# Kernel optimization log

Measured on AMD Instinct MI355X. Metric: run time of the kernel, lower is better.

The kernel has to match this reference:

```python
import jax, jax.numpy as jnp
import numpy as np

B, N, T, H = 32, 512, 3, 8
F_IN, F_HID, F_OUT = 768, 64, 64
NEG_SLOPE = 0.2
NEG_INF = -1e9


def setup_inputs() -> dict:
    key = jax.random.key(0)
    ks = jax.random.split(key, 16)
    s = 0.05
    emb = jax.random.normal(ks[0], (B, N, F_IN), jnp.float32)
    adj = jax.random.randint(ks[1], (B, N, N), 0, 2).astype(jnp.int32)
    adj = adj.at[:, jnp.arange(N), jnp.arange(N)].set(1)  # self loops so no empty rows
    vt_idx = jax.random.randint(ks[2], (B, N), 0, T)
    v_types = jax.nn.one_hot(vt_idx, T, dtype=jnp.float32)
    # layer 1 GAT params: per-type weights [T,H,f_in,f_out]
    w1 = jax.random.normal(ks[3], (T, H, F_IN, F_HID), jnp.float32) * s
    a_src1 = jax.random.normal(ks[4], (H, F_HID), jnp.float32) * s
    a_dst1 = jax.random.normal(ks[5], (H, F_HID), jnp.float32) * s
    b1 = jnp.zeros((F_HID,), jnp.float32)
    # layer 2 GAT (single head, f_in = H*F_HID)
    w2 = jax.random.normal(ks[6], (T, 1, H * F_HID, F_OUT), jnp.float32) * s
    a_src2 = jax.random.normal(ks[7], (1, F_OUT), jnp.float32) * s
    a_dst2 = jax.random.normal(ks[8], (1, F_OUT), jnp.float32) * s
    b2 = jnp.zeros((F_OUT,), jnp.float32)
    # MLP classifier: fc1 d->3d, fc2 3d->d, fc3 d->2
    fc1_w = jax.random.normal(ks[9], (F_OUT, 3 * F_OUT), jnp.float32) * s
    fc1_b = jnp.zeros((3 * F_OUT,), jnp.float32)
    fc2_w = jax.random.normal(ks[10], (3 * F_OUT, F_OUT), jnp.float32) * s
    fc2_b = jnp.zeros((F_OUT,), jnp.float32)
    fc3_w = jax.random.normal(ks[11], (F_OUT, 2), jnp.float32) * s
    fc3_b = jnp.zeros((2,), jnp.float32)
    return dict(emb=emb, adj=adj, v_types=v_types,
                w1=w1, a_src1=a_src1, a_dst1=a_dst1, b1=b1,
                w2=w2, a_src2=a_src2, a_dst2=a_dst2, b2=b2,
                fc1_w=fc1_w, fc1_b=fc1_b, fc2_w=fc2_w, fc2_b=fc2_b,
                fc3_w=fc3_w, fc3_b=fc3_b)


def _leaky_relu(x):
    return jnp.where(x >= 0, x, NEG_SLOPE * x)


def _gat(h, adj_mask, vt, w, a_src, a_dst, bias):
    # h: [B,N,f_in], vt: [B,N,T] one-hot, w: [T,Hd,f_in,f_out]
    # per-type projection then select node's type
    hpt = jnp.einsum('bni,thio->bntho', h, w)          # [B,N,T,Hd,f_out]
    hp = jnp.einsum('bnt,bntho->bnho', vt, hpt)        # [B,N,Hd,f_out]
    src = jnp.einsum('bnho,ho->bhn', hp, a_src)        # [B,Hd,N]
    dst = jnp.einsum('bnho,ho->bhn', hp, a_dst)
    e = _leaky_relu(src[:, :, :, None] + dst[:, :, None, :])  # [B,Hd,N,N]
    e = jnp.where(adj_mask[:, None, :, :], e, NEG_INF)
    attn = jax.nn.softmax(e, axis=-1)                  # attn_dropout=0.0 -> identity
    out = jnp.einsum('bhnm,bmho->bhno', attn, hp) + bias
    return out                                         # [B,Hd,N,f_out]


def reference(emb, adj, v_types, w1, a_src1, a_dst1, b1,
              w2, a_src2, a_dst2, b2,
              fc1_w, fc1_b, fc2_w, fc2_b, fc3_w, fc3_b):
    adj_mask = adj > 0
    x = _gat(emb, adj_mask, v_types, w1, a_src1, a_dst1, b1)    # [B,H,N,F_HID]
    x = jnp.transpose(x, (0, 2, 1, 3)).reshape(B, N, H * F_HID)  # concat heads
    x = jax.nn.elu(x)                                            # dropout: eval mode (identity)
    x = _gat(x, adj_mask, v_types, w2, a_src2, a_dst2, b2)       # [B,1,N,F_OUT]
    x = jax.nn.elu(x)
    x = x[:, 0, :, :]                                            # squeeze head dim -> [B,N,F_OUT]
    left = x[:, 0, :]
    right = x[:, 1, :]
    v = left * right
    v = jax.nn.relu(v @ fc1_w + fc1_b)
    v = jax.nn.relu(v @ fc2_w + fc2_b)
    scores = v @ fc3_w + fc3_b
    return jax.nn.log_softmax(scores, axis=1)
```

## Files before the change

kernel.cpp:

```cpp
#include <hip/hip_runtime.h>

#define BB   32
#define NN   512
#define NH   8
#define FIN  768
#define FHID 64
#define NROWS (BB*NN)

typedef __attribute__((ext_vector_type(8))) short bf16x8;
typedef __attribute__((ext_vector_type(4))) short s16x4;
typedef __attribute__((ext_vector_type(4))) float f32x4;
typedef unsigned long long u64;
typedef unsigned short u16;
typedef long i64;

__device__ __forceinline__ float lrelu_f(float s){ return fmaxf(s, 0.2f*s); }
__device__ __forceinline__ float elu_f(float s){ return s > 0.f ? s : expm1f(s); }
__device__ __forceinline__ short f2bf(float f){
  unsigned u = __float_as_uint(f);
  return (short)((u + 0x7fffu + ((u >> 16) & 1u)) >> 16);
}
__device__ __forceinline__ float bf2f(short s){
  return __uint_as_float(((unsigned)(u16)s) << 16);
}
__device__ __forceinline__ unsigned cvt_pk_bf16(float lo, float hi){
  unsigned r;
  asm("v_cvt_pk_bf16_f32 %0, %1, %2" : "=v"(r) : "v"(lo), "v"(hi));
  return r;
}
__device__ __forceinline__ float exp2_fast(float x){
  float r;
  asm("v_exp_f32 %0, %1" : "=v"(r) : "v"(x));
  return r;
}
__device__ __forceinline__ unsigned cvt_pk_fp8(float lo, float hi){
  return (unsigned)__builtin_amdgcn_cvt_pk_fp8_f32(lo, hi, 0, false);
}
__device__ __forceinline__ void gll16(const void* g, void* l){
  __builtin_amdgcn_global_load_lds(
      (const __attribute__((address_space(1))) void*)g,
      (__attribute__((address_space(3))) void*)l, 16, 0, 0);
}

__global__ __launch_bounds__(256) void prep_kernel(
    const int* __restrict__ adj,
    u64* __restrict__ maskw)
{
  int row  = blockIdx.x * 4 + (threadIdx.x >> 6);
  int lane = threadIdx.x & 63;
  const int* arow = adj + (long)row * NN;
  #pragma unroll
  for (int w = 0; w < 8; ++w) {
    u64 bal = __ballot(arow[w*64 + lane] > 0);
    if (lane == 0) maskw[(long)row*8 + w] = bal;
  }
}

__global__ __launch_bounds__(256) void rowlist_kernel(
    const float* __restrict__ vt,
    int* __restrict__ rowlist, int* __restrict__ counts)
{
  __shared__ int lc[3];
  __shared__ int lbase[3];
  int tid = threadIdx.x;
  int row = blockIdx.x * 256 + tid;
  if (tid < 3) lc[tid] = 0;
  __syncthreads();
  const float* v = vt + (long)row*3;
  int t = v[1] > 0.5f ? 1 : (v[2] > 0.5f ? 2 : 0);
  int p = atomicAdd(&lc[t], 1);
  __syncthreads();
  if (tid < 3) lbase[tid] = atomicAdd(&counts[tid], lc[tid]);
  __syncthreads();
  rowlist[t*NROWS + lbase[t] + p] = row;
}

__global__ __launch_bounds__(256) void conv_w(
    const float* __restrict__ w1, const float* __restrict__ w2,
    u16* __restrict__ w1t, u16* __restrict__ w2t)
{
  __shared__ float tile[64][68];
  int bid = blockIdx.x, tid = threadIdx.x;
  const float* src; u16* dst; int K;
  if (bid < 24) { src = w1 + (long)bid*768*64; dst = w1t + (long)bid*64*768; K = 768; }
  else { int t = bid - 24; src = w2 + (long)t*512*64; dst = w2t + (long)t*64*512; K = 512; }
  int kq = blockIdx.y;
  int kstart = kq * (K >> 2), kend = kstart + (K >> 2);

  for (int k0 = kstart; k0 < kend; k0 += 64) {
    __syncthreads();
    #pragma unroll
    for (int i = 0; i < 4; ++i) {
      int kk = i*16 + (tid >> 4);
      int oo = (tid & 15) * 4;
      float4 v = *(const float4*)(src + (long)(k0 + kk)*64 + oo);
      *(float4*)&tile[kk][oo] = v;
    }
    __syncthreads();
    int o = tid >> 2, kp = (tid & 3) * 16;
    unsigned pk[8];
    #pragma unroll
    for (int j = 0; j < 8; ++j)
      pk[j] = cvt_pk_bf16(tile[kp + 2*j][o], tile[kp + 2*j + 1][o]);
    u16* d = dst + (long)o*K + k0 + kp;
    #pragma unroll
    for (int j = 0; j < 8; ++j) *(unsigned*)(d + 2*j) = pk[j];
    __syncthreads();
  }
}

__global__ __launch_bounds__(256) void retile_w1(
    const u16* __restrict__ w1t, u16* __restrict__ w1tt)
{
  int thb = blockIdx.x;
  int kiter = blockIdx.y;
  int t = thb >> 2, hb = thb & 3;
  int tid = threadIdx.x;
  u16* dst = w1tt + ((long)thb*24 + kiter)*4096;
  #pragma unroll
  for (int c = 0; c < 2; ++c) {
    int u = c*256 + tid;
    int kg = u >> 7, col = u & 127;
    int head = hb*2 + (col >> 6), o = col & 63;
    int k = kiter*32 + kg*8;
    const u16* s = w1t + (((long)t*8 + head)*64 + o)*768 + k;
    *(bf16x8*)(dst + u*8) = *(const bf16x8*)s;
  }
}

__global__ __launch_bounds__(256) void gemm1_mfma(
    const float* __restrict__ emb,
    const u16* __restrict__ w1tt,
    const int* __restrict__ rowlist, const int* __restrict__ counts,
    u16* __restrict__ hp1b)
{
  int i   = blockIdx.x;
  int t   = i / 352;
  int r   = i - t*352;
  int cnt = counts[t];
  int xcd = r & 7;
  int q   = r >> 3;
  int hb  = q & 3;
  int rb  = (q >> 2) * 8 + xcd;
  int r0  = rb * 64;
  if (r0 >= cnt) return;

  __shared__ short aT[2][4*66*8];
  __shared__ short bT[2][4096];
  __shared__ int rowsS[64];

  int tid = threadIdx.x;
  if (tid < 64) {
    int rr = r0 + tid;
    rowsS[tid] = (rr < cnt) ? rowlist[t*NROWS + rr] : -1;
  }
  __syncthreads();

  int ar = tid >> 2, ac = tid & 3;
  int sg = rowsS[ar]; if (sg < 0) sg = rowsS[0];
  const float* aP = emb + (long)sg*768;

  const u16* bBase = w1tt + ((long)(t*4 + hb)*24)*4096;

  int wv = tid >> 6, l = tid & 63;
  int wr = wv >> 1, wc = wv & 1;
  int l15 = l & 15, lg = l >> 4;

  int aw0 = (( (ac>>1)     )*66 + ar)*8 + (ac&1)*4;
  int aw1 = (( 2 + (ac>>1) )*66 + ar)*8 + (ac&1)*4;

  f32x4 acc[2][4];
  #pragma unroll
  for (int fr = 0; fr < 2; ++fr)
    #pragma unroll
    for (int cf = 0; cf < 4; ++cf) acc[fr][cf] = (f32x4){0.f,0.f,0.f,0.f};

  gll16(bBase + tid*8,        &bT[0][tid*8]);
  gll16(bBase + (256+tid)*8,  &bT[0][(256+tid)*8]);
  float4 rA0 = *(const float4*)(aP + ac*4);
  float4 rA1 = *(const float4*)(aP + 16 + ac*4);
  {
    unsigned lo0 = cvt_pk_bf16(rA0.x, rA0.y), hi0 = cvt_pk_bf16(rA0.z, rA0.w);
    unsigned lo1 = cvt_pk_bf16(rA1.x, rA1.y), hi1 = cvt_pk_bf16(rA1.z, rA1.w);
    *(uint2*)&aT[0][aw0] = make_uint2(lo0, hi0);
    *(uint2*)&aT[0][aw1] = make_uint2(lo1, hi1);
  }
  rA0 = *(const float4*)(aP + 32 + ac*4);
  rA1 = *(const float4*)(aP + 48 + ac*4);
  __syncthreads();

  int cur = 0;
  for (int kiter = 0; kiter < 24; ++kiter) {
    if (kiter < 23) {
      const u16* bsrc = bBase + (long)(kiter+1)*4096;
      gll16(bsrc + tid*8,       &bT[cur^1][tid*8]);
      gll16(bsrc + (256+tid)*8, &bT[cur^1][(256+tid)*8]);
    }
    bf16x8 af_[2], bf_[4];
    #pragma unroll
    for (int fr = 0; fr < 2; ++fr)
      af_[fr] = *(const bf16x8*)&aT[cur][(lg*66 + wr*32 + fr*16 + l15)*8];
    #pragma unroll
    for (int cf = 0; cf < 4; ++cf)
      bf_[cf] = *(const bf16x8*)&bT[cur][(lg*128 + wc*64 + cf*16 + l15)*8];
    #pragma unroll
    for (int fr = 0; fr < 2; ++fr)
      #pragma unroll
      for (int cf = 0; cf < 4; ++cf)
        acc[fr][cf] = __builtin_amdgcn_mfma_f32_16x16x32_bf16(af_[fr], bf_[cf], acc[fr][cf], 0, 0, 0);
    if (kiter < 23) {
      unsigned lo0 = cvt_pk_bf16(rA0.x, rA0.y), hi0 = cvt_pk_bf16(rA0.z, rA0.w);
      unsigned lo1 = cvt_pk_bf16(rA1.x, rA1.y), hi1 = cvt_pk_bf16(rA1.z, rA1.w);
      *(uint2*)&aT[cur^1][aw0] = make_uint2(lo0, hi0);
      *(uint2*)&aT[cur^1][aw1] = make_uint2(lo1, hi1);
      if (kiter < 22) {
        rA0 = *(const float4*)(aP + (kiter+2)*32 + ac*4);
        rA1 = *(const float4*)(aP + (kiter+2)*32 + 16 + ac*4);
      }
    }
    __syncthreads();
    cur ^= 1;
  }

  #pragma unroll
  for (int fr = 0; fr < 2; ++fr) {
    #pragma unroll
    for (int r4 = 0; r4 < 4; ++r4) {
      int rloc = wr*32 + fr*16 + lg*4 + r4;
      int rg = rowsS[rloc];
      if (rg < 0) continue;
      long obase = ((long)(rg >> 9) * 8) * 32768 + (long)(rg & 511) * 64;
      #pragma unroll
      for (int cf = 0; cf < 4; ++cf) {
        int c = wc*64 + cf*16 + l15;
        hp1b[obase + (long)(hb*2 + (c >> 6))*32768 + (c & 63)] = (u16)f2bf(acc[fr][cf][r4]);
      }
    }
  }
}

__global__ __launch_bounds__(256) void gemm2_mfma(
    const u16* __restrict__ xbf,
    const u16* __restrict__ w2t,
    const int* __restrict__ rowlist, const int* __restrict__ counts,
    float* __restrict__ hp2)
{
  int i   = blockIdx.x;
  int t   = i >> 8;
  int cnt = counts[t];
  int r0  = (i & 255) * 64;
  if (r0 >= cnt) return;

  __shared__ short aT[4*66*8];
  __shared__ short bT[4*66*8];
  __shared__ int rowsS[64];

  int tid = threadIdx.x;
  if (tid < 64) {
    int rr = r0 + tid;
    rowsS[tid] = (rr < cnt) ? rowlist[t*NROWS + rr] : -1;
  }
  __syncthreads();

  int ar = tid >> 2, ac = tid & 3;
  int sg = rowsS[ar]; if (sg < 0) sg = rowsS[0];
  long apart = ((long)(sg >> 9) * 8) * 32768 + (long)(sg & 511) * 64;

  int colb = tid >> 2, off = tid & 3;
  const u16* bP = w2t + ((long)t*64 + colb)*512;

  int wv = tid >> 6, l = tid & 63;
  int l15 = l & 15, lg = l >> 4;

  f32x4 acc[4];
  #pragma unroll
  for (int cf = 0; cf < 4; ++cf) acc[cf] = (f32x4){0.f,0.f,0.f,0.f};

  int ka0 = ac*8;
  bf16x8 ra = *(const bf16x8*)(xbf + apart + (long)(ka0 >> 6)*32768 + (ka0 & 63));
  bf16x8 rb = *(const bf16x8*)(bP + off*8);

  for (int k0 = 0; k0 < 512; k0 += 32) {
    __syncthreads();
    *(bf16x8*)&aT[(ac*66 + ar)*8]   = ra;
    *(bf16x8*)&bT[(off*66 + colb)*8] = rb;
    __syncthreads();
    if (k0 + 32 < 512) {
      int kn = k0 + 32 + ac*8;
      ra = *(const bf16x8*)(xbf + apart + (long)(kn >> 6)*32768 + (kn & 63));
      rb = *(const bf16x8*)(bP + k0 + 32 + off*8);
    }
    bf16x8 af, bfr[4];
    af = *(const bf16x8*)&aT[(lg*66 + wv*16 + l15)*8];
    #pragma unroll
    for (int cf = 0; cf < 4; ++cf)
      bfr[cf] = *(const bf16x8*)&bT[(lg*66 + cf*16 + l15)*8];
    #pragma unroll
    for (int cf = 0; cf < 4; ++cf)
      acc[cf] = __builtin_amdgcn_mfma_f32_16x16x32_bf16(af, bfr[cf], acc[cf], 0, 0, 0);
  }

  #pragma unroll
  for (int r4 = 0; r4 < 4; ++r4) {
    int rloc = wv*16 + lg*4 + r4;
    int rg = rowsS[rloc];
    if (rg < 0) continue;
    #pragma unroll
    for (int cf = 0; cf < 4; ++cf)
      hp2[(long)rg*64 + cf*16 + l15] = acc[cf][r4];
  }
}

__global__ __launch_bounds__(1024) void gat1_attn(
    const u16* __restrict__ hp1b, const u64* __restrict__ maskw,
    const float* __restrict__ a_src, const float* __restrict__ a_dst,
    const float* __restrict__ b1, u16* __restrict__ xbf)
{
  extern __shared__ char smc[];
  char*  hpTf = smc;
  char*  pSf  = smc + 33792;
  float* srcS = (float*)(smc + 67584);
  float* dstS = (float*)(smc + 69632);
  float* asS  = (float*)(smc + 71680);
  float* adS  = (float*)(smc + 71936);
  float* rcpS = (float*)(smc + 72192);

  const float LOG2E = 1.4426950408889634f;

  int bid = blockIdx.x;
  int bh = bid >> 1, qh = bid & 1;
  int b = bh >> 3, h = bh & 7;
  int tid = threadIdx.x;

  if (tid < 64) asS[tid] = a_src[h*64 + tid];
  else if (tid < 128) adS[tid - 64] = a_dst[h*64 + (tid - 64)];
  __syncthreads();

  {
    int m = tid >> 1, half = tid & 1;
    int koct = m >> 3, kin = m & 7;
    const u16* hpRow = hp1b + ((long)bh*NN + m)*64 + half*32;
    float ps = 0.f, pd = 0.f;
    #pragma unroll
    for (int qq = 0; qq < 4; ++qq) {
      bf16x8 hv = *(const bf16x8*)(hpRow + qq*8);
      int o0 = half*32 + qq*8;
      #pragma unroll
      for (int j = 0; j < 8; ++j) {
        float f = bf2f(hv[j]);
        ps += f * asS[o0 + j];
        pd += f * adS[o0 + j];
        hpTf[(koct*66 + o0 + j)*8 + kin] = (char)(cvt_pk_fp8(f, f) & 0xffu);
      }
    }
    ps += __shfl_xor(ps, 1);
    pd += __shfl_xor(pd, 1);
    if ((tid & 1) == 0) { srcS[m] = ps * LOG2E; dstS[m] = pd * LOG2E; }
  }
  __syncthreads();

  int wv = tid >> 6, lane = tid & 63;
  int l15 = lane & 15, lg = lane >> 4;
  int cgl = wv >> 2, nt = wv & 3;
  int o_out = nt*16 + l15;
  float bb  = b1[o_out];

  float2 dst2[4];
  #pragma unroll
  for (int jj = 0; jj < 4; ++jj)
    dst2[jj] = *(const float2*)&dstS[jj*128 + 2*lane];
  int wsel = lane >> 5;
  unsigned sh = (unsigned)((2*lane) & 63);
  int pbase = ((lane >> 2)*66)*8 + 2*(lane & 3);

  for (int s = 0; s < 4; ++s) {
    int sup = qh*4 + s;
    #pragma unroll
    for (int rr = 0; rr < 4; ++rr) {
      int rloc = wv*4 + rr;
      int row  = sup*64 + rloc;
      float srcv = srcS[row];
      const u64* mrow = maskw + ((long)(b*NN + row))*8;
      float lsum = 0.f;
      #pragma unroll
      for (int jj = 0; jj < 4; ++jj) {
        u64 w = mrow[jj*2 + wsel];
        unsigned bits = (unsigned)(w >> sh) & 3u;
        float s0 = srcv + dst2[jj].x;
        float s1 = srcv + dst2[jj].y;
        float p0 = (bits & 1u) ? exp2_fast(lrelu_f(s0)) : 0.f;
        float p1 = (bits & 2u) ? exp2_fast(lrelu_f(s1)) : 0.f;
        lsum += p0 + p1;
        *(u16*)&pSf[(jj*16*66)*8 + pbase + rloc*8] = (u16)cvt_pk_fp8(p0, p1);
      }
      #pragma unroll
      for (int mk = 1; mk <= 32; mk <<= 1) lsum += __shfl_xor(lsum, mk);
      if (lane == 0) rcpS[rloc] = 1.f / lsum;
    }
    __syncthreads();

    f32x4 acc = {0.f, 0.f, 0.f, 0.f};
    #pragma unroll
    for (int ks = 0; ks < 16; ++ks) {
      int koct = ks*4 + lg;
      i64 af = *(const i64*)&pSf [(koct*66 + cgl*16 + l15)*8];
      i64 bf = *(const i64*)&hpTf[(koct*66 + nt*16  + l15)*8];
      acc = __builtin_amdgcn_mfma_f32_16x16x32_fp8_fp8(af, bf, acc, 0, 0, 0);
    }
    #pragma unroll
    for (int reg = 0; reg < 4; ++reg) {
      int rloc = cgl*16 + lg*4 + reg;
      int row  = sup*64 + rloc;
      float v = elu_f(acc[reg] * rcpS[rloc] + bb);
      xbf[((long)bh*NN + row)*64 + o_out] = (u16)f2bf(v);
    }
    __syncthreads();
  }
}

__global__ __launch_bounds__(256) void gat2_final(
    const float* __restrict__ hp2, const u64* __restrict__ maskw,
    const float* __restrict__ a_src2, const float* __restrict__ a_dst2,
    const float* __restrict__ b2,
    const float* __restrict__ fc1_w, const float* __restrict__ fc1_b,
    const float* __restrict__ fc2_w, const float* __restrict__ fc2_b,
    const float* __restrict__ fc3_w, const float* __restrict__ fc3_b,
    float* __restrict__ out)
{
  extern __shared__ float sm[];
  float* hpS  = sm;
  float* dstS = hpS + 32768;
  float* srcS = dstS + 512;
  float* pS   = srcS + 512;
  float* redS = pS + 512;
  float* outS = redS + 256;
  float* vS   = outS + 128;
  float* y1S  = vS + 64;
  float* redM = y1S + 192;
  float4* hpS4 = (float4*)hpS;

  int b = blockIdx.x;
  int tid = threadIdx.x;
  int og = tid & 15, m16 = tid >> 4;

  for (int it = 0; it < 32; ++it) {
    int fi = it*256 + tid;
    int m = fi >> 4, o4 = fi & 15;
    hpS4[m*16 + o4] = *(const float4*)(hp2 + (long)(b*NN + m)*64 + o4*4);
  }
  __syncthreads();

  float4 as4 = *(const float4*)(a_src2 + og*4);
  float4 ad4 = *(const float4*)(a_dst2 + og*4);
  for (int it = 0; it < 32; ++it) {
    int m = it*16 + m16;
    float4 hv = hpS4[m*16 + og];
    float ls = hv.x*as4.x + hv.y*as4.y + hv.z*as4.z + hv.w*as4.w;
    float ld = hv.x*ad4.x + hv.y*ad4.y + hv.z*ad4.z + hv.w*ad4.w;
    #pragma unroll
    for (int mk = 1; mk <= 8; mk <<= 1) {
      ls += __shfl_xor(ls, mk);
      ld += __shfl_xor(ld, mk);
    }
    if (og == 0) { srcS[m] = ls; dstS[m] = ld; }
  }
  __syncthreads();

  for (int n = 0; n < 2; ++n) {
    float srcv = srcS[n];
    const u64* mrow = maskw + (long)(b*NN + n)*8;
    int m0 = tid, m1 = tid + 256;
    u64 w0 = mrow[m0 >> 6], w1 = mrow[m1 >> 6];
    float s0 = srcv + dstS[m0], s1 = srcv + dstS[m1];
    float e0 = ((w0 >> (m0 & 63)) & 1ull) ? lrelu_f(s0) : -1.0e9f;
    float e1 = ((w1 >> (m1 & 63)) & 1ull) ? lrelu_f(s1) : -1.0e9f;
    float emax = fmaxf(e0, e1);
    #pragma unroll
    for (int mk = 1; mk <= 32; mk <<= 1) emax = fmaxf(emax, __shfl_xor(emax, mk));
    if ((tid & 63) == 0) redM[tid >> 6] = emax;
    __syncthreads();
    emax = fmaxf(fmaxf(redM[0], redM[1]), fmaxf(redM[2], redM[3]));
    float p0 = __expf(e0 - emax), p1 = __expf(e1 - emax);
    pS[m0] = p0; pS[m1] = p1;
    float lsum = p0 + p1;
    #pragma unroll
    for (int mk = 1; mk <= 32; mk <<= 1) lsum += __shfl_xor(lsum, mk);
    if ((tid & 63) == 0) redM[4 + (tid >> 6)] = lsum;
    __syncthreads();
    float rcp = 1.f / (redM[4] + redM[5] + redM[6] + redM[7]);

    float4 acc = make_float4(0.f,0.f,0.f,0.f);
    for (int mm = 0; mm < 32; ++mm) {
      int m = mm*16 + m16;
      float4 hv = hpS4[m*16 + og];
      float p = pS[m];
      acc.x += hv.x*p; acc.y += hv.y*p; acc.z += hv.z*p; acc.w += hv.w*p;
    }
    acc.x += __shfl_xor(acc.x, 16); acc.y += __shfl_xor(acc.y, 16);
    acc.z += __shfl_xor(acc.z, 16); acc.w += __shfl_xor(acc.w, 16);
    acc.x += __shfl_xor(acc.x, 32); acc.y += __shfl_xor(acc.y, 32);
    acc.z += __shfl_xor(acc.z, 32); acc.w += __shfl_xor(acc.w, 32);
    __syncthreads();
    if ((tid & 63) < 16) ((float4*)redS)[(tid >> 6)*16 + (tid & 15)] = acc;
    __syncthreads();
    if (tid < 16) {
      float4 s = make_float4(0.f,0.f,0.f,0.f);
      #pragma unroll
      for (int w = 0; w < 4; ++w) {
        float4 v = ((float4*)redS)[w*16 + tid];
        s.x += v.x; s.y += v.y; s.z += v.z; s.w += v.w;
      }
      float4 bv = *(const float4*)(b2 + tid*4);
      outS[n*64 + tid*4 + 0] = elu_f(s.x*rcp + bv.x);
      outS[n*64 + tid*4 + 1] = elu_f(s.y*rcp + bv.y);
      outS[n*64 + tid*4 + 2] = elu_f(s.z*rcp + bv.z);
      outS[n*64 + tid*4 + 3] = elu_f(s.w*rcp + bv.w);
    }
    __syncthreads();
  }

  if (tid < 64) vS[tid] = outS[tid] * outS[64 + tid];
  __syncthreads();
  if (tid < 192) {
    float a = fc1_b[tid];
    for (int o = 0; o < 64; ++o) a += vS[o]*fc1_w[o*192 + tid];
    y1S[tid] = a > 0.f ? a : 0.f;
  }
  __syncthreads();
  if (tid < 64) {
    float a = fc2_b[tid];
    for (int j = 0; j < 192; ++j) a += y1S[j]*fc2_w[j*64 + tid];
    vS[tid] = a > 0.f ? a : 0.f;
  }
  __syncthreads();
  if (tid == 0) {
    float t0 = fc3_b[0], t1 = fc3_b[1];
    for (int k = 0; k < 64; ++k) {
      float y = vS[k];
      t0 += y*fc3_w[k*2 + 0];
      t1 += y*fc3_w[k*2 + 1];
    }
    float mx = fmaxf(t0, t1);
    float lse = mx + logf(__expf(t0 - mx) + __expf(t1 - mx));
    out[b*2 + 0] = t0 - lse;
    out[b*2 + 1] = t1 - lse;
  }
}

extern "C" void kernel_launch(void* const* d_in, const int* in_sizes, int n_in,
                              void* d_out, int out_size, void* d_ws, size_t ws_size,
                              hipStream_t stream) {
  const float* emb    = (const float*)d_in[0];
  const int*   adj    = (const int*)d_in[1];
  const float* vt     = (const float*)d_in[2];
  const float* w1     = (const float*)d_in[3];
  const float* a_src1 = (const float*)d_in[4];
  const float* a_dst1 = (const float*)d_in[5];
  const float* b1     = (const float*)d_in[6];
  const float* w2     = (const float*)d_in[7];
  const float* a_src2 = (const float*)d_in[8];
  const float* a_dst2 = (const float*)d_in[9];
  const float* b2     = (const float*)d_in[10];
  const float* fc1_w  = (const float*)d_in[11];
  const float* fc1_b  = (const float*)d_in[12];
  const float* fc2_w  = (const float*)d_in[13];
  const float* fc2_b  = (const float*)d_in[14];
  const float* fc3_w  = (const float*)d_in[15];
  const float* fc3_b  = (const float*)d_in[16];

  char* ws = (char*)d_ws;
  int* counts  = (int*)ws;
  int* rowlist = (int*)(ws + 4096);
  u64* maskw   = (u64*)(ws + 204800);
  u16* w1t     = (u16*)(ws + 1310720);
  u16* w2t     = (u16*)(ws + 3670016);
  u16* hp1b    = (u16*)(ws + 3932160);
  float* hp2   = (float*)(ws + 20709376);
  u16* w1tt    = (u16*)(ws + 20709376);
  u16* xbf     = (u16*)(ws + 24903680);

  hipMemsetAsync(counts, 0, 16, stream);
  prep_kernel<<<NROWS/4, 256, 0, stream>>>(adj, maskw);
  rowlist_kernel<<<NROWS/256, 256, 0, stream>>>(vt, rowlist, counts);
  conv_w<<<dim3(27, 4), 256, 0, stream>>>(w1, w2, w1t, w2t);
  retile_w1<<<dim3(12, 24), 256, 0, stream>>>(w1t, w1tt);

  gemm1_mfma<<<dim3(1056), 256, 0, stream>>>(emb, w1tt, rowlist, counts, hp1b);

  size_t sm1 = 72448;
  gat1_attn<<<BB*NH*2, 1024, sm1, stream>>>(hp1b, maskw, a_src1, a_dst1, b1, xbf);

  gemm2_mfma<<<dim3(768), 256, 0, stream>>>(xbf, w2t, rowlist, counts, hp2);

  size_t sm2 = (size_t)(32768 + 512 + 512 + 512 + 256 + 128 + 64 + 192 + 8) * 4;
  gat2_final<<<BB, 256, sm2, stream>>>(hp2, maskw, a_src2, a_dst2, b2,
                                       fc1_w, fc1_b, fc2_w, fc2_b, fc3_w, fc3_b,
                                       (float*)d_out);
}
```

Baseline: 143.3 us.

## Fuse w1 retiling into conversion and double gemm1 row tile to 128

The weight conversion kernel now writes w1 directly in the MFMA-tiled layout, which removes the separate retile_w1 launch and its extra global round trip. gemm1 now processes 128 rows per block instead of 64, with each wave computing 4x4 MFMA fragments, so each B tile is reused across twice as many rows and the grid shrinks from 1056 to 516 blocks. The XCD-aware block swizzle is dropped. The costs are higher register and LDS use per block, fewer blocks to fill the GPU, and wider per-thread A loads.

```diff
diff --git a/kernel.cpp b/kernel.cpp
--- a/kernel.cpp
+++ b/kernel.cpp
@@ -77,13 +77,13 @@
 
 __global__ __launch_bounds__(256) void conv_w(
     const float* __restrict__ w1, const float* __restrict__ w2,
-    u16* __restrict__ w1t, u16* __restrict__ w2t)
+    u16* __restrict__ w1tt, u16* __restrict__ w2t)
 {
   __shared__ float tile[64][68];
   int bid = blockIdx.x, tid = threadIdx.x;
-  const float* src; u16* dst; int K;
-  if (bid < 24) { src = w1 + (long)bid*768*64; dst = w1t + (long)bid*64*768; K = 768; }
-  else { int t = bid - 24; src = w2 + (long)t*512*64; dst = w2t + (long)t*64*512; K = 512; }
+  const float* src; int K;
+  if (bid < 24) { src = w1 + (long)bid*768*64; K = 768; }
+  else { src = w2 + (long)(bid - 24)*512*64; K = 512; }
   int kq = blockIdx.y;
   int kstart = kq * (K >> 2), kend = kstart + (K >> 2);
 
@@ -102,29 +102,21 @@
     #pragma unroll
     for (int j = 0; j < 8; ++j)
       pk[j] = cvt_pk_bf16(tile[kp + 2*j][o], tile[kp + 2*j + 1][o]);
-    u16* d = dst + (long)o*K + k0 + kp;
-    #pragma unroll
-    for (int j = 0; j < 8; ++j) *(unsigned*)(d + 2*j) = pk[j];
-    __syncthreads();
-  }
-}
-
-__global__ __launch_bounds__(256) void retile_w1(
-    const u16* __restrict__ w1t, u16* __restrict__ w1tt)
-{
-  int thb = blockIdx.x;
-  int kiter = blockIdx.y;
-  int t = thb >> 2, hb = thb & 3;
-  int tid = threadIdx.x;
-  u16* dst = w1tt + ((long)thb*24 + kiter)*4096;
-  #pragma unroll
-  for (int c = 0; c < 2; ++c) {
-    int u = c*256 + tid;
-    int kg = u >> 7, col = u & 127;
-    int head = hb*2 + (col >> 6), o = col & 63;
-    int k = kiter*32 + kg*8;
-    const u16* s = w1t + (((long)t*8 + head)*64 + o)*768 + k;
-    *(bf16x8*)(dst + u*8) = *(const bf16x8*)s;
+    if (bid < 24) {
+      int t = bid >> 3, head = bid & 7;
+      int hb = head >> 1, col = (head & 1)*64 + o;
+      int k = k0 + kp;
+      int kiter = k >> 5, kg = (k >> 3) & 3;
+      u16* base = w1tt + (((long)(t*4 + hb)*24 + kiter)*4096) + kg*1024 + col*8;
+      *(bf16x8*)base          = *(bf16x8*)&pk[0];
+      *(bf16x8*)(base + 1024) = *(bf16x8*)&pk[4];
+    } else {
+      int t = bid - 24;
+      u16* d = w2t + ((long)t*64 + o)*512 + k0 + kp;
+      #pragma unroll
+      for (int j = 0; j < 8; ++j) *(unsigned*)(d + 2*j) = pk[j];
+    }
+    __syncthreads();
   }
 }
 
@@ -135,30 +127,28 @@
     u16* __restrict__ hp1b)
 {
   int i   = blockIdx.x;
-  int t   = i / 352;
-  int r   = i - t*352;
+  int t   = i / 172;
+  int r   = i - t*172;
   int cnt = counts[t];
-  int xcd = r & 7;
-  int q   = r >> 3;
-  int hb  = q & 3;
-  int rb  = (q >> 2) * 8 + xcd;
-  int r0  = rb * 64;
+  int hb  = r & 3;
+  int rb  = r >> 2;
+  int r0  = rb * 128;
   if (r0 >= cnt) return;
 
-  __shared__ short aT[2][4*66*8];
+  __shared__ short aT[2][4*130*8];
   __shared__ short bT[2][4096];
-  __shared__ int rowsS[64];
+  __shared__ int rowsS[128];
 
   int tid = threadIdx.x;
-  if (tid < 64) {
+  if (tid < 128) {
     int rr = r0 + tid;
     rowsS[tid] = (rr < cnt) ? rowlist[t*NROWS + rr] : -1;
   }
   __syncthreads();
 
-  int ar = tid >> 2, ac = tid & 3;
+  int ar = tid >> 1, ac = tid & 1;
   int sg = rowsS[ar]; if (sg < 0) sg = rowsS[0];
-  const float* aP = emb + (long)sg*768;
+  const float* aP = emb + (long)sg*768 + ac*16;
 
   const u16* bBase = w1tt + ((long)(t*4 + hb)*24)*4096;
 
@@ -166,27 +156,33 @@
   int wr = wv >> 1, wc = wv & 1;
   int l15 = l & 15, lg = l >> 4;
 
-  int aw0 = (( (ac>>1)     )*66 + ar)*8 + (ac&1)*4;
-  int aw1 = (( 2 + (ac>>1) )*66 + ar)*8 + (ac&1)*4;
-
-  f32x4 acc[2][4];
+  int aw0 = ((ac*2    )*130 + ar)*8;
+  int aw1 = ((ac*2 + 1)*130 + ar)*8;
+
+  f32x4 acc[4][4];
   #pragma unroll
-  for (int fr = 0; fr < 2; ++fr)
+  for (int fr = 0; fr < 4; ++fr)
     #pragma unroll
     for (int cf = 0; cf < 4; ++cf) acc[fr][cf] = (f32x4){0.f,0.f,0.f,0.f};
 
   gll16(bBase + tid*8,        &bT[0][tid*8]);
   gll16(bBase + (256+tid)*8,  &bT[0][(256+tid)*8]);
-  float4 rA0 = *(const float4*)(aP + ac*4);
-  float4 rA1 = *(const float4*)(aP + 16 + ac*4);
+  float4 rA0 = *(const float4*)(aP);
+  float4 rA1 = *(const float4*)(aP + 4);
+  float4 rA2 = *(const float4*)(aP + 8);
+  float4 rA3 = *(const float4*)(aP + 12);
   {
-    unsigned lo0 = cvt_pk_bf16(rA0.x, rA0.y), hi0 = cvt_pk_bf16(rA0.z, rA0.w);
-    unsigned lo1 = cvt_pk_bf16(rA1.x, rA1.y), hi1 = cvt_pk_bf16(rA1.z, rA1.w);
-    *(uint2*)&aT[0][aw0] = make_uint2(lo0, hi0);
-    *(uint2*)&aT[0][aw1] = make_uint2(lo1, hi1);
-  }
-  rA0 = *(const float4*)(aP + 32 + ac*4);
-  rA1 = *(const float4*)(aP + 48 + ac*4);
+    unsigned p0 = cvt_pk_bf16(rA0.x, rA0.y), p1 = cvt_pk_bf16(rA0.z, rA0.w);
+    unsigned p2 = cvt_pk_bf16(rA1.x, rA1.y), p3 = cvt_pk_bf16(rA1.z, rA1.w);
+    unsigned p4 = cvt_pk_bf16(rA2.x, rA2.y), p5 = cvt_pk_bf16(rA2.z, rA2.w);
+    unsigned p6 = cvt_pk_bf16(rA3.x, rA3.y), p7 = cvt_pk_bf16(rA3.z, rA3.w);
+    *(uint4*)&aT[0][aw0] = make_uint4(p0, p1, p2, p3);
+    *(uint4*)&aT[0][aw1] = make_uint4(p4, p5, p6, p7);
+  }
+  rA0 = *(const float4*)(aP + 32);
+  rA1 = *(const float4*)(aP + 36);
+  rA2 = *(const float4*)(aP + 40);
+  rA3 = *(const float4*)(aP + 44);
   __syncthreads();
 
   int cur = 0;
@@ -196,26 +192,31 @@
       gll16(bsrc + tid*8,       &bT[cur^1][tid*8]);
       gll16(bsrc + (256+tid)*8, &bT[cur^1][(256+tid)*8]);
     }
-    bf16x8 af_[2], bf_[4];
-    #pragma unroll
-    for (int fr = 0; fr < 2; ++fr)
-      af_[fr] = *(const bf16x8*)&aT[cur][(lg*66 + wr*32 + fr*16 + l15)*8];
+    bf16x8 af_[4], bf_[4];
+    #pragma unroll
+    for (int fr = 0; fr < 4; ++fr)
+      af_[fr] = *(const bf16x8*)&aT[cur][(lg*130 + wr*64 + fr*16 + l15)*8];
     #pragma unroll
     for (int cf = 0; cf < 4; ++cf)
       bf_[cf] = *(const bf16x8*)&bT[cur][(lg*128 + wc*64 + cf*16 + l15)*8];
     #pragma unroll
-    for (int fr = 0; fr < 2; ++fr)
+    for (int fr = 0; fr < 4; ++fr)
       #pragma unroll
       for (int cf = 0; cf < 4; ++cf)
         acc[fr][cf] = __builtin_amdgcn_mfma_f32_16x16x32_bf16(af_[fr], bf_[cf], acc[fr][cf], 0, 0, 0);
     if (kiter < 23) {
-      unsigned lo0 = cvt_pk_bf16(rA0.x, rA0.y), hi0 = cvt_pk_bf16(rA0.z, rA0.w);
-      unsigned lo1 = cvt_pk_bf16(rA1.x, rA1.y), hi1 = cvt_pk_bf16(rA1.z, rA1.w);
-      *(uint2*)&aT[cur^1][aw0] = make_uint2(lo0, hi0);
-      *(uint2*)&aT[cur^1][aw1] = make_uint2(lo1, hi1);
+      unsigned p0 = cvt_pk_bf16(rA0.x, rA0.y), p1 = cvt_pk_bf16(rA0.z, rA0.w);
+      unsigned p2 = cvt_pk_bf16(rA1.x, rA1.y), p3 = cvt_pk_bf16(rA1.z, rA1.w);
+      unsigned p4 = cvt_pk_bf16(rA2.x, rA2.y), p5 = cvt_pk_bf16(rA2.z, rA2.w);
+      unsigned p6 = cvt_pk_bf16(rA3.x, rA3.y), p7 = cvt_pk_bf16(rA3.z, rA3.w);
+      *(uint4*)&aT[cur^1][aw0] = make_uint4(p0, p1, p2, p3);
+      *(uint4*)&aT[cur^1][aw1] = make_uint4(p4, p5, p6, p7);
       if (kiter < 22) {
-        rA0 = *(const float4*)(aP + (kiter+2)*32 + ac*4);
-        rA1 = *(const float4*)(aP + (kiter+2)*32 + 16 + ac*4);
+        const float* ap2 = aP + (kiter+2)*32;
+        rA0 = *(const float4*)(ap2);
+        rA1 = *(const float4*)(ap2 + 4);
+        rA2 = *(const float4*)(ap2 + 8);
+        rA3 = *(const float4*)(ap2 + 12);
       }
     }
     __syncthreads();
@@ -223,10 +224,10 @@
   }
 
   #pragma unroll
-  for (int fr = 0; fr < 2; ++fr) {
+  for (int fr = 0; fr < 4; ++fr) {
     #pragma unroll
     for (int r4 = 0; r4 < 4; ++r4) {
-      int rloc = wr*32 + fr*16 + lg*4 + r4;
+      int rloc = wr*64 + fr*16 + lg*4 + r4;
       int rg = rowsS[rloc];
       if (rg < 0) continue;
       long obase = ((long)(rg >> 9) * 8) * 32768 + (long)(rg & 511) * 64;
@@ -572,20 +573,18 @@
   int* counts  = (int*)ws;
   int* rowlist = (int*)(ws + 4096);
   u64* maskw   = (u64*)(ws + 204800);
-  u16* w1t     = (u16*)(ws + 1310720);
   u16* w2t     = (u16*)(ws + 3670016);
   u16* hp1b    = (u16*)(ws + 3932160);
   float* hp2   = (float*)(ws + 20709376);
-  u16* w1tt    = (u16*)(ws + 20709376);
+  u16* w1tt    = (u16*)(ws + 1310720);
   u16* xbf     = (u16*)(ws + 24903680);
 
   hipMemsetAsync(counts, 0, 16, stream);
   prep_kernel<<<NROWS/4, 256, 0, stream>>>(adj, maskw);
   rowlist_kernel<<<NROWS/256, 256, 0, stream>>>(vt, rowlist, counts);
-  conv_w<<<dim3(27, 4), 256, 0, stream>>>(w1, w2, w1t, w2t);
-  retile_w1<<<dim3(12, 24), 256, 0, stream>>>(w1t, w1tt);
-
-  gemm1_mfma<<<dim3(1056), 256, 0, stream>>>(emb, w1tt, rowlist, counts, hp1b);
+  conv_w<<<dim3(27, 4), 256, 0, stream>>>(w1, w2, w1tt, w2t);
+
+  gemm1_mfma<<<dim3(516), 256, 0, stream>>>(emb, w1tt, rowlist, counts, hp1b);
 
   size_t sm1 = 72448;
   gat1_attn<<<BB*NH*2, 1024, sm1, stream>>>(hp1b, maskw, a_src1, a_dst1, b1, xbf);
```

Result: slower. 156.7 us (+9.3%).
